# Optimization experiments

Hardware: AMD Instinct MI355X
Metric: run time of the kernel (lower is better)

## Reference

```python
import jax, jax.numpy as jnp
import numpy as np

N, R, K, B, M, D = 300000, 1200, 20, 256, 50, 100


def setup_inputs() -> dict:
    key = jax.random.key(0)
    ks = jax.random.split(key, 16)
    w = lambda k, s: jax.random.normal(k, s, dtype=jnp.float32) * 0.1
    return {
        "node_embedding": jax.random.normal(ks[0], (N, D), dtype=jnp.float32),
        "relation_embedding": jax.random.normal(ks[1], (R, D), dtype=jnp.float32),
        "origin_embedding": jax.random.normal(ks[2], (B, D), dtype=jnp.float32),
        "graph_embedding": jax.random.normal(ks[3], (B, D), dtype=jnp.float32),
        "actor_w1": w(ks[4], (3 * D, D)), "actor_b1": jnp.zeros((D,), jnp.float32),
        "actor_w2": w(ks[5], (D, D)), "actor_b2": jnp.zeros((D,), jnp.float32),
        "actor_w3": w(ks[6], (D, 1)), "actor_b3": jnp.zeros((1,), jnp.float32),
        "critic_w1": w(ks[7], (3 * D, D)), "critic_b1": jnp.zeros((D,), jnp.float32),
        "critic_w2": w(ks[8], (D, D)), "critic_b2": jnp.zeros((D,), jnp.float32),
        "critic_w3": w(ks[9], (D, 1)), "critic_b3": jnp.zeros((1,), jnp.float32),
        "entity_adj": jax.random.randint(ks[10], (N, K), 0, N, dtype=jnp.int64),
        "relation_adj": jax.random.randint(ks[11], (N, K), 0, R, dtype=jnp.int64),
        "nodes": jax.random.randint(ks[12], (B, M), 0, N, dtype=jnp.int64),
    }


def _head(x, w1, b1, w2, b2, w3, b3):
    # tanh(L1) -> tanh(L2) -> sigmoid(L3), per Net.forward
    h = jnp.tanh(x @ w1 + b1)
    h = jnp.tanh(h @ w2 + b2)
    return jax.nn.sigmoid(h @ w3 + b3)


def reference(node_embedding, relation_embedding, origin_embedding, graph_embedding,
              actor_w1, actor_b1, actor_w2, actor_b2, actor_w3, actor_b3,
              critic_w1, critic_b1, critic_w2, critic_b2, critic_w3, critic_b3,
              entity_adj, relation_adj, nodes):
    # one-hop KG expansion: gather neighbor entity / relation ids of frontier nodes
    neigh_ids = entity_adj[nodes]          # [B, M, K]
    rel_ids = relation_adj[nodes]          # [B, M, K]
    neigh = node_embedding[neigh_ids]      # [B, M, K, D]
    rel = relation_embedding[rel_ids]      # [B, M, K, D]
    action = jnp.concatenate([neigh, rel], axis=-1)                    # [B, M, K, 2D]
    state = jnp.broadcast_to(graph_embedding[:, None, None, :], neigh.shape)
    x = jnp.concatenate([state, action], axis=-1)                      # [B, M, K, 3D]
    act_probs = _head(x, actor_w1, actor_b1, actor_w2, actor_b2, actor_w3, actor_b3)
    q_actions = _head(x, critic_w1, critic_b1, critic_w2, critic_b2, critic_w3, critic_b3)
    # get_sim_reward_batch: dot_rewards + updated graph embedding
    b, m, k, d = neigh.shape
    flat_node = neigh.reshape(b, m * k, d)                             # [B, M*K, D]
    ge = graph_embedding[:, None, :]                                   # [B, 1, D]
    dot_rewards = jax.nn.softmax(
        jnp.sum(origin_embedding[:, None, :] * (ge + flat_node), axis=-1), axis=-1)
    new_graph_embedding = ge + flat_node                               # [B, M*K, D]
    return (act_probs, q_actions, dot_rewards, new_graph_embedding)
```

## Files before the change

### kernel.cpp

```cpp
#include <hip/hip_runtime.h>
#include <hip/hip_bf16.h>

#define NND 300000
#define RR 1200
#define KADJ 20
#define BB 256
#define MM 50
#define DD 100
#define ROWS (BB*MM*KADJ)
#define MKJ (MM*KADJ)
#define N1P 208
#define K1S 8
#define NT1 7
#define NT2 7
#define K2S 4
#define H1S 136

typedef __attribute__((ext_vector_type(8))) short short8;
typedef __attribute__((ext_vector_type(4))) float f32x4;

__device__ inline unsigned short f2bf(float f) {
  union { float f; unsigned u; } v; v.f = f;
  return (unsigned short)((v.u + 0x7FFFu + ((v.u >> 16) & 1u)) >> 16);
}
__device__ inline unsigned pkbf2(float x, float y) {
  __hip_bfloat162 p = __float22bfloat162_rn(make_float2(x, y));
  unsigned u; __builtin_memcpy(&u, &p, 4); return u;
}
__device__ inline float fast_tanh(float x) {
  float e = __builtin_amdgcn_exp2f(x * 2.885390082f);
  float r = __builtin_amdgcn_rcpf(e + 1.f);
  return __builtin_fmaf(-2.f, r, 1.f);
}
__device__ inline float fast_sigmoid(float x) {
  float e = __builtin_amdgcn_exp2f(x * -1.442695041f);
  return __builtin_amdgcn_rcpf(1.f + e);
}

__global__ __launch_bounds__(256) void k_prep(
    const float* __restrict__ gemb,
    const float* __restrict__ aw1, const float* __restrict__ ab1,
    const float* __restrict__ cw1, const float* __restrict__ cb1,
    const float* __restrict__ aw2, const float* __restrict__ cw2,
    short* __restrict__ wf1, short* __restrict__ wf2, float* __restrict__ G1) {
  int t = blockIdx.x * blockDim.x + threadIdx.x;
  if (t < 57344) {
    int j = t & 7, l = (t >> 3) & 63, f = t >> 9;
    int ks = f & 7, r2 = f >> 3;
    int nt = r2 % 7, h = r2 / 7;
    int kp = ks * 32 + ((l >> 4) * 8) + j;
    int n = nt * 16 + (l & 15);
    float v = 0.f;
    if (n < DD) {
      const float* w1 = h ? cw1 : aw1;
      if (kp < DD) v = w1[(DD + kp) * DD + n];
      else if (kp >= 128 && kp < 228) v = w1[(200 + kp - 128) * DD + n];
    }
    wf1[t] = (short)f2bf(v);
    return;
  }
  int t2 = t - 57344;
  if (t2 < 28672) {
    int j = t2 & 7, l = (t2 >> 3) & 63, f = t2 >> 9;
    int ks = f & 3, r2 = f >> 2;
    int nt = r2 % 7, h = r2 / 7;
    int k = ks * 32 + ((l >> 4) * 8) + j;
    int n = nt * 16 + (l & 15);
    float v = 0.f;
    if (k < DD && n < DD) v = (h ? cw2 : aw2)[k * DD + n];
    wf2[t2] = (short)f2bf(v);
    return;
  }
  int t3 = t2 - 28672;
  if (t3 < BB * N1P) {
    int b = t3 / N1P, n = t3 % N1P;
    float acc = 0.f;
    if (n < 200) {
      const float* w1 = (n < DD) ? aw1 : cw1;
      const float* b1 = (n < DD) ? ab1 : cb1;
      int jj = (n < DD) ? n : n - DD;
      acc = b1[jj];
      for (int d = 0; d < DD; ++d) acc += gemb[b * DD + d] * w1[d * DD + jj];
    }
    G1[t3] = acc;
  }
}

__global__ __launch_bounds__(256) void k_soft(float* __restrict__ dr) {
  __shared__ float red[4];
  int b = blockIdx.x, tid = threadIdx.x;
  int lane = tid & 63, w = tid >> 6;
  float* p = dr + (size_t)b * MKJ;
  float v[4], mx = -1e30f;
  #pragma unroll
  for (int i = 0; i < 4; ++i) {
    int j = tid + i * 256;
    v[i] = (j < MKJ) ? p[j] : -1e30f;
    mx = fmaxf(mx, v[i]);
  }
  #pragma unroll
  for (int off = 32; off; off >>= 1) mx = fmaxf(mx, __shfl_xor(mx, off, 64));
  if (lane == 0) red[w] = mx;
  __syncthreads();
  mx = fmaxf(fmaxf(red[0], red[1]), fmaxf(red[2], red[3]));
  float e[4], se = 0.f;
  #pragma unroll
  for (int i = 0; i < 4; ++i) {
    e[i] = __expf(v[i] - mx);
    if (tid + i * 256 < MKJ) se += e[i];
  }
  #pragma unroll
  for (int off = 32; off; off >>= 1) se += __shfl_xor(se, off, 64);
  __syncthreads();
  if (lane == 0) red[w] = se;
  __syncthreads();
  se = red[0] + red[1] + red[2] + red[3];
  float inv = 1.f / se;
  #pragma unroll
  for (int i = 0; i < 4; ++i) {
    int j = tid + i * 256;
    if (j < MKJ) p[j] = e[i] * inv;
  }
}

template<bool FUSE>
__global__ __launch_bounds__(256, 5) void k_all(
    const float* __restrict__ nemb, const float* __restrict__ remb,
    const float* __restrict__ oemb, const float* __restrict__ gemb,
    const int* __restrict__ eadj, const int* __restrict__ radj,
    const int* __restrict__ nodes,
    const short* __restrict__ wf1, const short* __restrict__ wf2,
    const float* __restrict__ G1,
    const float* __restrict__ ab2, const float* __restrict__ cb2,
    const float* __restrict__ aw3, const float* __restrict__ ab3,
    const float* __restrict__ cw3, const float* __restrict__ cb3,
    float* __restrict__ outA, float* __restrict__ outQ,
    float* __restrict__ dots, float* __restrict__ outNG) {
  __shared__ uint4 WB[512];
  __shared__ unsigned short H1[64 * H1S];
  __shared__ float G1s[224], b2s[224], w3s[224];
  __shared__ float gs[128], os[128];
  __shared__ int nidS[64], ridS[64];

  int hid = blockIdx.x;
  int x = hid & 15, b = hid >> 4;
  int tid = threadIdx.x;
  int lane = tid & 63, w = tid >> 6, ln = lane & 15, lg = lane >> 4;

  if (tid < 64) {
    int row = x * 64 + tid;
    int rc = row < MKJ ? row : MKJ - 1;
    int m = rc / KADJ, kk = rc - m * KADJ;
    int v = nodes[b * MM + m];
    nidS[tid] = eadj[v * KADJ + kk];
    ridS[tid] = radj[v * KADJ + kk];
  }
  for (int i = tid; i < 224; i += 256) {
    int h = i / 112, n = i - h * 112;
    G1s[i] = (n < DD) ? G1[b * N1P + h * DD + n] : 0.f;
    b2s[i] = (n < DD) ? (h ? cb2[n] : ab2[n]) : 0.f;
    w3s[i] = (n < DD) ? (h ? cw3[n] : aw3[n]) : 0.f;
  }
  if (FUSE) {
    for (int i = tid; i < 128; i += 256) {
      gs[i] = (i < DD) ? gemb[b * DD + i] : 0.f;
      os[i] = (i < DD) ? oemb[b * DD + i] : 0.f;
    }
  }
  __syncthreads();

  short8 a1[8];
  int myrow = w * 16 + ln;
  int grow = x * 64 + myrow;
  bool vrow = grow < MKJ;
  float pp = 0.f;
  {
    const float* nrow = nemb + (size_t)nidS[myrow] * DD;
    const float* rrow = remb + (size_t)ridS[myrow] * DD;
    #pragma unroll
    for (int ks = 0; ks < 8; ++ks) {
      const float* src = (ks < 4) ? nrow : rrow;
      int cb = (ks & 3) * 32 + lg * 8;
      float4 lo = make_float4(0.f,0.f,0.f,0.f), hi = lo;
      if (cb <= 96) lo = *(const float4*)(src + cb);
      if (cb + 4 <= 96) hi = *(const float4*)(src + cb + 4);
      union { short8 s; unsigned u[4]; } fr;
      fr.u[0] = pkbf2(lo.x, lo.y); fr.u[1] = pkbf2(lo.z, lo.w);
      fr.u[2] = pkbf2(hi.x, hi.y); fr.u[3] = pkbf2(hi.z, hi.w);
      a1[ks] = fr.s;
      if (FUSE && ks < 4 && cb <= 96) {
        pp += os[cb+0]*(lo.x+gs[cb+0]) + os[cb+1]*(lo.y+gs[cb+1]) +
              os[cb+2]*(lo.z+gs[cb+2]) + os[cb+3]*(lo.w+gs[cb+3]);
        if (cb + 4 <= 96)
          pp += os[cb+4]*(hi.x+gs[cb+4]) + os[cb+5]*(hi.y+gs[cb+5]) +
                os[cb+6]*(hi.z+gs[cb+6]) + os[cb+7]*(hi.w+gs[cb+7]);
      }
    }
  }

  if (FUSE) {
    pp += __shfl_xor(pp, 16, 64);
    pp += __shfl_xor(pp, 32, 64);
    if (lg == 0 && vrow) dots[(size_t)b * MKJ + grow] = pp;

    #pragma unroll
    for (int ks = 0; ks < 4; ++ks) {
      int col = (ks * 32 + lg * 8) ^ ((myrow & 7) << 3);
      *(short8*)&H1[myrow * H1S + col] = a1[ks];
    }
    __syncthreads();

    const size_t ngbase = ((size_t)b * MKJ + (size_t)x * 64) * DD;
    for (int q = tid; q < 1600; q += 256) {
      int fidx = q * 4;
      int row = fidx / DD;
      int col = fidx - row * DD;
      if (x * 64 + row < MKJ) {
        int sc = ((col & ~7) ^ ((row & 7) << 3)) + (col & 7);
        unsigned long long d = *(const unsigned long long*)&H1[row * H1S + sc];
        f32x4 t;
        #pragma unroll
        for (int e = 0; e < 4; ++e) {
          unsigned u = (unsigned)((d >> (16 * e)) & 0xFFFFull) << 16;
          float v; __builtin_memcpy(&v, &u, 4);
          t[e] = v + gs[col + e];
        }
        __builtin_nontemporal_store(t, (f32x4*)(outNG + ngbase + fidx));
      }
    }
  }

  float b3v[2] = {ab3[0], cb3[0]};
  float* outs[2] = {outA, outQ};

  for (int h = 0; h < 2; ++h) {
    const char* wf1b = (const char*)wf1 + (size_t)h * 57344;
    __syncthreads();
    {
      const uint4* src = (const uint4*)wf1b;
      WB[tid] = src[tid];
      WB[tid + 256] = src[tid + 256];
    }
    __syncthreads();
    for (int nt = 0; nt < NT1; ++nt) {
      uint4 s0, s1;
      if (nt < NT1 - 1) {
        const uint4* src = (const uint4*)(wf1b + (size_t)(nt + 1) * 8192);
        s0 = src[tid];
        s1 = src[tid + 256];
      }
      int n = nt * 16 + ln;
      float g = G1s[h * 112 + n];
      f32x4 acc = {g, g, g, g};
      #pragma unroll
      for (int ks = 0; ks < K1S; ++ks) {
        short8 bw = *(const short8*)&WB[ks * 64 + lane];
        acc = __builtin_amdgcn_mfma_f32_16x16x32_bf16(a1[ks], bw, acc, 0, 0, 0);
      }
      if (n < DD) {
        #pragma unroll
        for (int r = 0; r < 4; ++r) {
          int row = w * 16 + lg * 4 + r;
          int csw = n ^ (((row >> 2) & 3) << 3);
          H1[row * H1S + csw] = f2bf(fast_tanh(acc[r]));
        }
      }
      if (nt < NT1 - 1) {
        __syncthreads();
        WB[tid] = s0;
        WB[tid + 256] = s1;
        __syncthreads();
      }
    }
    __syncthreads();

    short8 a2[4];
    {
      int sw = ((myrow >> 2) & 3) << 3;
      #pragma unroll
      for (int ks = 0; ks < K2S; ++ks) {
        int col = (ks * 32 + lg * 8) ^ sw;
        a2[ks] = *(const short8*)&H1[myrow * H1S + col];
      }
      union { short8 s; unsigned short us[8]; } m; m.s = a2[3];
      int cb = 96 + lg * 8;
      #pragma unroll
      for (int q = 0; q < 8; ++q) if (cb + q >= DD) m.us[q] = 0;
      a2[3] = m.s;
    }

    const char* wf2b = (const char*)wf2 + (size_t)h * 28672;
    WB[tid] = ((const uint4*)wf2b)[tid];
    __syncthreads();
    float part[4] = {0.f, 0.f, 0.f, 0.f};
    for (int nt = 0; nt < NT2; ++nt) {
      uint4 s0;
      if (nt < NT2 - 1)
        s0 = ((const uint4*)(wf2b + (size_t)(nt + 1) * 4096))[tid];
      f32x4 acc = {0.f, 0.f, 0.f, 0.f};
      #pragma unroll
      for (int ks = 0; ks < K2S; ++ks) {
        short8 bw = *(const short8*)&WB[ks * 64 + lane];
        acc = __builtin_amdgcn_mfma_f32_16x16x32_bf16(a2[ks], bw, acc, 0, 0, 0);
      }
      int n = nt * 16 + ln;
      float b2v = b2s[h * 112 + n];
      float w3v = w3s[h * 112 + n];
      #pragma unroll
      for (int r = 0; r < 4; ++r)
        part[r] += fast_tanh(acc[r] + b2v) * w3v;
      if (nt < NT2 - 1) {
        __syncthreads();
        WB[tid] = s0;
        __syncthreads();
      }
    }
    #pragma unroll
    for (int r = 0; r < 4; ++r) {
      float s = part[r];
      s += __shfl_xor(s, 1, 64); s += __shfl_xor(s, 2, 64);
      s += __shfl_xor(s, 4, 64); s += __shfl_xor(s, 8, 64);
      if (ln == 0) {
        int row = x * 64 + w * 16 + lg * 4 + r;
        if (row < MKJ) outs[h][(size_t)b * MKJ + row] = fast_sigmoid(s + b3v[h]);
      }
    }
  }
}

__global__ __launch_bounds__(1024) void k_rewards(
    const float* __restrict__ nemb, const float* __restrict__ oemb,
    const float* __restrict__ gemb,
    const int* __restrict__ eadj, const int* __restrict__ nodes,
    float* __restrict__ outDR, float* __restrict__ outNG) {
  __shared__ float dots[MKJ];
  __shared__ float red[16];
  int b = blockIdx.x;
  int tid = threadIdx.x;
  int lane = tid & 63, w = tid >> 6;
  int d1 = lane + 64;
  float o0 = oemb[b * DD + lane];
  float g0 = gemb[b * DD + lane];
  float o1 = (d1 < DD) ? oemb[b * DD + d1] : 0.f;
  float g1 = (d1 < DD) ? gemb[b * DD + d1] : 0.f;
  for (int j = w; j < MKJ; j += 16) {
    int m = j / KADJ, kk = j - m * KADJ;
    int v = nodes[b * MM + m];
    int nid = eadj[v * KADJ + kk];
    const float* nr = nemb + (size_t)nid * DD;
    float s0 = g0 + nr[lane];
    float s1 = (d1 < DD) ? (g1 + nr[d1]) : 0.f;
    float* ngr = outNG + ((long long)b * MKJ + j) * DD;
    ngr[lane] = s0;
    if (d1 < DD) ngr[d1] = s1;
    float p = o0 * s0 + o1 * s1;
    p += __shfl_xor(p, 1, 64); p += __shfl_xor(p, 2, 64); p += __shfl_xor(p, 4, 64);
    p += __shfl_xor(p, 8, 64); p += __shfl_xor(p, 16, 64); p += __shfl_xor(p, 32, 64);
    if (lane == 0) dots[j] = p;
  }
  __syncthreads();
  float mx = -1e30f;
  for (int j = tid; j < MKJ; j += 1024) mx = fmaxf(mx, dots[j]);
  for (int off = 32; off; off >>= 1) mx = fmaxf(mx, __shfl_xor(mx, off, 64));
  if (lane == 0) red[w] = mx;
  __syncthreads();
  mx = red[0];
  #pragma unroll
  for (int i = 1; i < 16; ++i) mx = fmaxf(mx, red[i]);
  float se = 0.f;
  for (int j = tid; j < MKJ; j += 1024) se += __expf(dots[j] - mx);
  for (int off = 32; off; off >>= 1) se += __shfl_xor(se, off, 64);
  __syncthreads();
  if (lane == 0) red[w] = se;
  __syncthreads();
  se = 0.f;
  #pragma unroll
  for (int i = 0; i < 16; ++i) se += red[i];
  float inv = 1.f / se;
  for (int j = tid; j < MKJ; j += 1024) outDR[b * MKJ + j] = __expf(dots[j] - mx) * inv;
}

extern "C" void kernel_launch(void* const* d_in, const int* in_sizes, int n_in,
                              void* d_out, int out_size, void* d_ws, size_t ws_size,
                              hipStream_t stream) {
  const float* nemb = (const float*)d_in[0];
  const float* remb = (const float*)d_in[1];
  const float* oemb = (const float*)d_in[2];
  const float* gemb = (const float*)d_in[3];
  const float* aw1 = (const float*)d_in[4];
  const float* ab1 = (const float*)d_in[5];
  const float* aw2 = (const float*)d_in[6];
  const float* ab2 = (const float*)d_in[7];
  const float* aw3 = (const float*)d_in[8];
  const float* ab3 = (const float*)d_in[9];
  const float* cw1 = (const float*)d_in[10];
  const float* cb1 = (const float*)d_in[11];
  const float* cw2 = (const float*)d_in[12];
  const float* cb2 = (const float*)d_in[13];
  const float* cw3 = (const float*)d_in[14];
  const float* cb3 = (const float*)d_in[15];
  const int* eadj = (const int*)d_in[16];
  const int* radj = (const int*)d_in[17];
  const int* nodes = (const int*)d_in[18];

  float* out = (float*)d_out;
  float* outA = out;
  float* outQ = out + ROWS;
  float* outDR = out + 2 * ROWS;
  float* outNG = out + 3 * ROWS;

  const size_t need = 385024;
  bool fuse = ws_size >= need;
  char* scratch = (char*)d_ws;
  if (!fuse) {
    scratch = (char*)(out + ((size_t)3 * ROWS + (size_t)ROWS * DD - need / 4));
  }
  short* wf1 = (short*)scratch;
  short* wf2 = (short*)(scratch + 114688);
  float* G1 = (float*)(scratch + 172032);

  k_prep<<<544, 256, 0, stream>>>(gemb, aw1, ab1, cw1, cb1, aw2, cw2, wf1, wf2, G1);
  if (fuse) {
    k_all<true><<<4096, 256, 0, stream>>>(nemb, remb, oemb, gemb, eadj, radj, nodes,
                                          wf1, wf2, G1, ab2, cb2, aw3, ab3, cw3, cb3,
                                          outA, outQ, outDR, outNG);
    k_soft<<<BB, 256, 0, stream>>>(outDR);
  } else {
    k_all<false><<<4096, 256, 0, stream>>>(nemb, remb, oemb, gemb, eadj, radj, nodes,
                                           wf1, wf2, G1, ab2, cb2, aw3, ab3, cw3, cb3,
                                           outA, outQ, outDR, outNG);
    k_rewards<<<BB, 1024, 0, stream>>>(nemb, oemb, gemb, eadj, nodes, outDR, outNG);
  }
}
```

Measured before the change: 121.2 us.

## Double rows per block to share weight staging across eight waves

The fused MLP kernel now runs 512-thread blocks that each process 128 rows instead of 64. Each staged weight tile in shared memory is therefore reused by twice as many waves, which halves the global-to-LDS weight traffic and barrier rounds per row. The first weight tile is also prefetched into registers before the new-graph-embedding store phase. The XOR swizzle on the layer-1 activation buffer is dropped. In exchange, the larger LDS footprint lowers how many blocks fit per CU, and the unswizzled layout may bring back LDS bank conflicts.

Measured after the change: 113.3 us. -6.5%, faster.

```diff
diff --git a/kernel.cpp b/kernel.cpp
--- a/kernel.cpp
+++ b/kernel.cpp
@@ -124,7 +124,7 @@
 }
 
 template<bool FUSE>
-__global__ __launch_bounds__(256, 5) void k_all(
+__global__ __launch_bounds__(512, 4) void k_all(
     const float* __restrict__ nemb, const float* __restrict__ remb,
     const float* __restrict__ oemb, const float* __restrict__ gemb,
     const int* __restrict__ eadj, const int* __restrict__ radj,
@@ -137,32 +137,32 @@
     float* __restrict__ outA, float* __restrict__ outQ,
     float* __restrict__ dots, float* __restrict__ outNG) {
   __shared__ uint4 WB[512];
-  __shared__ unsigned short H1[64 * H1S];
+  __shared__ unsigned short H1[128 * H1S];
   __shared__ float G1s[224], b2s[224], w3s[224];
   __shared__ float gs[128], os[128];
-  __shared__ int nidS[64], ridS[64];
+  __shared__ int nidS[128], ridS[128];
 
   int hid = blockIdx.x;
-  int x = hid & 15, b = hid >> 4;
+  int x = hid & 7, b = hid >> 3;
   int tid = threadIdx.x;
   int lane = tid & 63, w = tid >> 6, ln = lane & 15, lg = lane >> 4;
 
-  if (tid < 64) {
-    int row = x * 64 + tid;
+  if (tid < 128) {
+    int row = x * 128 + tid;
     int rc = row < MKJ ? row : MKJ - 1;
     int m = rc / KADJ, kk = rc - m * KADJ;
     int v = nodes[b * MM + m];
     nidS[tid] = eadj[v * KADJ + kk];
     ridS[tid] = radj[v * KADJ + kk];
   }
-  for (int i = tid; i < 224; i += 256) {
+  for (int i = tid; i < 224; i += 512) {
     int h = i / 112, n = i - h * 112;
     G1s[i] = (n < DD) ? G1[b * N1P + h * DD + n] : 0.f;
     b2s[i] = (n < DD) ? (h ? cb2[n] : ab2[n]) : 0.f;
     w3s[i] = (n < DD) ? (h ? cw3[n] : aw3[n]) : 0.f;
   }
   if (FUSE) {
-    for (int i = tid; i < 128; i += 256) {
+    for (int i = tid; i < 128; i += 512) {
       gs[i] = (i < DD) ? gemb[b * DD + i] : 0.f;
       os[i] = (i < DD) ? oemb[b * DD + i] : 0.f;
     }
@@ -171,7 +171,7 @@
 
   short8 a1[8];
   int myrow = w * 16 + ln;
-  int grow = x * 64 + myrow;
+  int grow = x * 128 + myrow;
   bool vrow = grow < MKJ;
   float pp = 0.f;
   {
@@ -198,6 +198,8 @@
     }
   }
 
+  uint4 p0 = ((const uint4*)wf1)[tid];
+
   if (FUSE) {
     pp += __shfl_xor(pp, 16, 64);
     pp += __shfl_xor(pp, 32, 64);
@@ -210,12 +212,12 @@
     }
     __syncthreads();
 
-    const size_t ngbase = ((size_t)b * MKJ + (size_t)x * 64) * DD;
-    for (int q = tid; q < 1600; q += 256) {
+    const size_t ngbase = ((size_t)b * MKJ + (size_t)x * 128) * DD;
+    for (int q = tid; q < 3200; q += 512) {
       int fidx = q * 4;
       int row = fidx / DD;
       int col = fidx - row * DD;
-      if (x * 64 + row < MKJ) {
+      if (x * 128 + row < MKJ) {
         int sc = ((col & ~7) ^ ((row & 7) << 3)) + (col & 7);
         unsigned long long d = *(const unsigned long long*)&H1[row * H1S + sc];
         f32x4 t;
@@ -228,6 +230,7 @@
         __builtin_nontemporal_store(t, (f32x4*)(outNG + ngbase + fidx));
       }
     }
+    __syncthreads();
   }
 
   float b3v[2] = {ab3[0], cb3[0]};
@@ -235,20 +238,17 @@
 
   for (int h = 0; h < 2; ++h) {
     const char* wf1b = (const char*)wf1 + (size_t)h * 57344;
-    __syncthreads();
-    {
-      const uint4* src = (const uint4*)wf1b;
-      WB[tid] = src[tid];
-      WB[tid + 256] = src[tid + 256];
+    if (h == 0) {
+      WB[tid] = p0;
+    } else {
+      __syncthreads();
+      WB[tid] = ((const uint4*)wf1b)[tid];
     }
     __syncthreads();
     for (int nt = 0; nt < NT1; ++nt) {
-      uint4 s0, s1;
-      if (nt < NT1 - 1) {
-        const uint4* src = (const uint4*)(wf1b + (size_t)(nt + 1) * 8192);
-        s0 = src[tid];
-        s1 = src[tid + 256];
-      }
+      uint4 s0;
+      if (nt < NT1 - 1)
+        s0 = ((const uint4*)(wf1b + (size_t)(nt + 1) * 8192))[tid];
       int n = nt * 16 + ln;
       float g = G1s[h * 112 + n];
       f32x4 acc = {g, g, g, g};
@@ -259,29 +259,22 @@
       }
       if (n < DD) {
         #pragma unroll
-        for (int r = 0; r < 4; ++r) {
-          int row = w * 16 + lg * 4 + r;
-          int csw = n ^ (((row >> 2) & 3) << 3);
-          H1[row * H1S + csw] = f2bf(fast_tanh(acc[r]));
-        }
+        for (int r = 0; r < 4; ++r)
+          H1[(w * 16 + lg * 4 + r) * H1S + n] = f2bf(fast_tanh(acc[r]));
       }
       if (nt < NT1 - 1) {
         __syncthreads();
         WB[tid] = s0;
-        WB[tid + 256] = s1;
         __syncthreads();
       }
     }
     __syncthreads();
 
     short8 a2[4];
+    #pragma unroll
+    for (int ks = 0; ks < K2S; ++ks)
+      a2[ks] = *(const short8*)&H1[myrow * H1S + ks * 32 + lg * 8];
     {
-      int sw = ((myrow >> 2) & 3) << 3;
-      #pragma unroll
-      for (int ks = 0; ks < K2S; ++ks) {
-        int col = (ks * 32 + lg * 8) ^ sw;
-        a2[ks] = *(const short8*)&H1[myrow * H1S + col];
-      }
       union { short8 s; unsigned short us[8]; } m; m.s = a2[3];
       int cb = 96 + lg * 8;
       #pragma unroll
@@ -290,12 +283,12 @@
     }
 
     const char* wf2b = (const char*)wf2 + (size_t)h * 28672;
-    WB[tid] = ((const uint4*)wf2b)[tid];
+    if (tid < 256) WB[tid] = ((const uint4*)wf2b)[tid];
     __syncthreads();
     float part[4] = {0.f, 0.f, 0.f, 0.f};
     for (int nt = 0; nt < NT2; ++nt) {
       uint4 s0;
-      if (nt < NT2 - 1)
+      if (nt < NT2 - 1 && tid < 256)
         s0 = ((const uint4*)(wf2b + (size_t)(nt + 1) * 4096))[tid];
       f32x4 acc = {0.f, 0.f, 0.f, 0.f};
       #pragma unroll
@@ -311,7 +304,7 @@
         part[r] += fast_tanh(acc[r] + b2v) * w3v;
       if (nt < NT2 - 1) {
         __syncthreads();
-        WB[tid] = s0;
+        if (tid < 256) WB[tid] = s0;
         __syncthreads();
       }
     }
@@ -321,10 +314,11 @@
       s += __shfl_xor(s, 1, 64); s += __shfl_xor(s, 2, 64);
       s += __shfl_xor(s, 4, 64); s += __shfl_xor(s, 8, 64);
       if (ln == 0) {
-        int row = x * 64 + w * 16 + lg * 4 + r;
+        int row = x * 128 + w * 16 + lg * 4 + r;
         if (row < MKJ) outs[h][(size_t)b * MKJ + row] = fast_sigmoid(s + b3v[h]);
       }
     }
+    __syncthreads();
   }
 }
 
@@ -421,12 +415,12 @@
 
   k_prep<<<544, 256, 0, stream>>>(gemb, aw1, ab1, cw1, cb1, aw2, cw2, wf1, wf2, G1);
   if (fuse) {
-    k_all<true><<<4096, 256, 0, stream>>>(nemb, remb, oemb, gemb, eadj, radj, nodes,
+    k_all<true><<<2048, 512, 0, stream>>>(nemb, remb, oemb, gemb, eadj, radj, nodes,
                                           wf1, wf2, G1, ab2, cb2, aw3, ab3, cw3, cb3,
                                           outA, outQ, outDR, outNG);
     k_soft<<<BB, 256, 0, stream>>>(outDR);
   } else {
-    k_all<false><<<4096, 256, 0, stream>>>(nemb, remb, oemb, gemb, eadj, radj, nodes,
+    k_all<false><<<2048, 512, 0, stream>>>(nemb, remb, oemb, gemb, eadj, radj, nodes,
                                            wf1, wf2, G1, ab2, cb2, aw3, ab3, cw3, cb3,
                                            outA, outQ, outDR, outNG);
     k_rewards<<<BB, 1024, 0, stream>>>(nemb, oemb, gemb, eadj, nodes, outDR, outNG);
```
